# Kernel optimization log

Measured on AMD Instinct MI355X. Metric: run time of the kernel, lower is better.

## Reference

```python
import jax, jax.numpy as jnp
import numpy as np

# ---- HashGrid config (tcnn defaults from module __init__) ----
N_LEVELS = 6
F = 2                      # n_features_per_level
T = 2 ** 19                # hashmap size
BASE = 16                  # base_resolution, per_level_scale=2.0
_RES = [BASE * (2 ** l) for l in range(N_LEVELS)]          # 16..512
_SIZES = [min(r ** 3, T) for r in _RES]                    # dense if grid fits
_OFFSETS = [0] + list(np.cumsum(_SIZES))
TOTAL_ENTRIES = int(_OFFSETS[-1])
_PRIMES = (1, 2654435761, 805459861)
BOX_R = 1.0
DIM_H = 64
DIM_IN = 3 + N_LEVELS * F


def hash_encode(xn, grid):
    """Multi-res hash-grid encoding. xn: [N,3] in [0,1]; grid: [TOTAL_ENTRIES, F]."""
    feats = []
    for l in range(N_LEVELS):
        res, size, off = _RES[l], _SIZES[l], _OFFSETS[l]
        dense = (res ** 3) <= T
        pos = xn * jnp.float32(res - 1) + 0.5          # tcnn: scale*x + 0.5
        pg = jnp.floor(pos)
        frac = pos - pg                                # [N,3]
        pgi = pg.astype(jnp.uint32)
        acc = jnp.zeros((xn.shape[0], F), xn.dtype)
        for corner in range(8):                        # trilinear, 8 corners
            cb = jnp.array([(corner >> d) & 1 for d in range(3)], dtype=jnp.uint32)
            c = pgi + cb                               # [N,3] corner coords
            w = jnp.prod(jnp.where(cb == 1, frac, 1.0 - frac), axis=-1)  # [N]
            if dense:
                c = jnp.minimum(c, jnp.uint32(res - 1))
                idx = c[:, 0] + c[:, 1] * jnp.uint32(res) + c[:, 2] * jnp.uint32(res * res)
            else:
                idx = ((c[:, 0] * jnp.uint32(_PRIMES[0]))
                       ^ (c[:, 1] * jnp.uint32(_PRIMES[1]))
                       ^ (c[:, 2] * jnp.uint32(_PRIMES[2]))) % jnp.uint32(size)
            acc = acc + w[:, None] * grid[jnp.uint32(off) + idx]
        feats.append(acc)
    return jnp.concatenate(feats, axis=-1)             # [N, 12]


def setup_inputs() -> dict:
    key = jax.random.key(0)
    k0, k1, k2 = jax.random.split(key, 3)
    N = 2_097_152
    x = jax.random.uniform(k0, (N, 3), jnp.float32, -1.0, 1.0)
    grid = jax.random.uniform(k1, (TOTAL_ENTRIES, F), jnp.float32, -1e-2, 1e-2)
    W0 = jax.random.normal(k2, (DIM_IN, DIM_H), jnp.float32) * float(np.sqrt(2.0 / DIM_H))
    b0 = jnp.zeros((DIM_H,), jnp.float32)
    W1 = jnp.full((DIM_H, 1), float(np.sqrt(np.pi / DIM_H)), jnp.float32)
    b1 = jnp.full((1,), -1.0, jnp.float32)             # -init_radius
    return {"x": x, "grid": grid, "W0": W0, "b0": b0, "W1": W1, "b1": b1}


def reference(x, grid, W0, b0, W1, b1):
    xn = (x + BOX_R) / (2.0 * BOX_R)                   # normalize to [0,1]
    f = hash_encode(xn, grid)                          # [N,12]
    h = jnp.concatenate([x, f], axis=-1)               # [N,15]
    h = jax.nn.relu(h @ W0 + b0)                       # [N,64]
    return h @ W1 + b1                                 # [N,1] scalar level s
```

## Files before the change

kernel.cpp:

```cpp
#include <hip/hip_runtime.h>


#define HP1 2654435761u
#define HP2 805459861u
#define HMASK ((1u << 19) - 1u)

typedef float v2f __attribute__((ext_vector_type(2)));

static __device__ __forceinline__ unsigned umin_(unsigned a, unsigned b) {
    return a < b ? a : b;
}

static __device__ __forceinline__ unsigned f2bf(float f) {
    unsigned u = __float_as_uint(f);
    return (u + 0x7fffu + ((u >> 16) & 1u)) >> 16;
}
static __device__ __forceinline__ float bf2f_lo(unsigned p) {
    return __uint_as_float((p & 0xffffu) << 16);
}
static __device__ __forceinline__ float bf2f_hi(unsigned p) {
    return __uint_as_float(p & 0xffff0000u);
}

static __device__ __forceinline__ v2f vmax0(v2f s) {
#if __has_builtin(__builtin_elementwise_max)
    return __builtin_elementwise_max(s, (v2f)0.0f);
#else
    v2f r; r.x = fmaxf(s.x, 0.0f); r.y = fmaxf(s.y, 0.0f); return r;
#endif
}

static __device__ __forceinline__ void hash_body(
    const float* __restrict__ x, const float2* __restrict__ tab,
    unsigned* __restrict__ feat, float scale, int N, int bid)
{
    const int gid = bid * 256 + threadIdx.x;
    if (gid >= N) return;

    const float px = __builtin_nontemporal_load(x + 3 * gid + 0);
    const float py = __builtin_nontemporal_load(x + 3 * gid + 1);
    const float pz = __builtin_nontemporal_load(x + 3 * gid + 2);

    const float p0 = fmaf((px + 1.0f) * 0.5f, scale, 0.5f);
    const float p1 = fmaf((py + 1.0f) * 0.5f, scale, 0.5f);
    const float p2 = fmaf((pz + 1.0f) * 0.5f, scale, 0.5f);
    const float g0 = floorf(p0), g1 = floorf(p1), g2 = floorf(p2);
    const float f0 = p0 - g0, f1 = p1 - g1, f2 = p2 - g2;
    const unsigned i0 = (unsigned)g0, i1 = (unsigned)g1, i2 = (unsigned)g2;

    const float wx[2] = {1.0f - f0, f0};
    const float wy[2] = {1.0f - f1, f1};
    const float wz[2] = {1.0f - f2, f2};
    const unsigned hy[2] = {i1 * HP1, (i1 + 1u) * HP1};
    const unsigned hz[2] = {i2 * HP2, (i2 + 1u) * HP2};

    float2 v0[4], v1[4];
    #pragma unroll
    for (int c = 0; c < 4; ++c) {
        const unsigned m = hy[c & 1] ^ hz[(c >> 1) & 1];
        const unsigned e0 = (i0 ^ m) & HMASK;
        const float4 q = *reinterpret_cast<const float4*>(
            reinterpret_cast<const float*>(tab) + 2u * (e0 & ~1u));
        const float2 qlo = make_float2(q.x, q.y);
        const float2 qhi = make_float2(q.z, q.w);
        const bool hi = (e0 & 1u) != 0u;
        v0[c] = hi ? qhi : qlo;
        v1[c] = hi ? qlo : qhi;
    }
    if (i0 & 1u) {
        #pragma unroll
        for (int c = 0; c < 4; ++c) {
            const unsigned e1 =
                ((i0 + 1u) ^ hy[c & 1] ^ hz[(c >> 1) & 1]) & HMASK;
            v1[c] = tab[e1];
        }
    }

    float a0 = 0.0f, a1 = 0.0f;
    #pragma unroll
    for (int c = 0; c < 4; ++c) {
        const float wyz = wy[c & 1] * wz[(c >> 1) & 1];
        const float w0 = wyz * wx[0], w1 = wyz * wx[1];
        a0 = fmaf(w0, v0[c].x, a0);
        a1 = fmaf(w0, v0[c].y, a1);
        a0 = fmaf(w1, v1[c].x, a0);
        a1 = fmaf(w1, v1[c].y, a1);
    }
    __builtin_nontemporal_store(f2bf(a0) | (f2bf(a1) << 16), feat + gid);
}

__global__ __launch_bounds__(256) void hash3_prep_kernel(
    const float* __restrict__ x, const float2* __restrict__ gtab,
    unsigned* __restrict__ feat0, int N,
    float* __restrict__ wt, unsigned* __restrict__ packed,
    unsigned* __restrict__ A2, unsigned* __restrict__ B2,
    const float* __restrict__ W0, const float* __restrict__ b0,
    const float* __restrict__ W1, const float* __restrict__ b1)
{
    const int nh = (int)gridDim.x - 64;
    if ((int)blockIdx.x >= nh) {
        const int pb = (int)blockIdx.x - nh;
        for (int t = pb * 256 + threadIdx.x; t < 36864; t += 64 * 256) {
            const float2 e = gtab[t];
            packed[t] = f2bf(e.x) | (f2bf(e.y) << 16);
        }
        const float2* g2 = gtab + 36864u;
        for (int t = pb * 256 + threadIdx.x; t < 262144; t += 64 * 256) {
            const float2 e = g2[t];
            A2[t] = f2bf(e.x) | (f2bf(e.y) << 16);
            const int xc = t & 63;
            const float2 en = g2[(xc == 63) ? t : t + 1];
            B2[t] = f2bf(en.x) | (f2bf(en.y) << 16);
        }
        if (pb == 0) {
            for (int t = threadIdx.x; t < 1024; t += 256) {
                const int j = t >> 4, i = t & 15;
                wt[t] = (i == 15) ? b0[j] : W0[i * 64 + j];
            }
            if (threadIdx.x < 64) wt[1024 + threadIdx.x] = W1[threadIdx.x];
            if (threadIdx.x == 0) wt[1088] = b1[0];
        }
        return;
    }
    hash_body(x, gtab + 299008u, feat0, 127.0f, N, (int)blockIdx.x);
}

__global__ __launch_bounds__(256) void hash_level_kernel(
    const float* __restrict__ x, const float2* __restrict__ tab,
    unsigned* __restrict__ feat, float scale, int N)
{
    hash_body(x, tab, feat, scale, N, (int)blockIdx.x);
}

static __device__ __forceinline__ void dense_level(
    const float2* __restrict__ tab, unsigned res,
    float xn0, float xn1, float xn2, float& o0, float& o1)
{
    const float scale = (float)(res - 1);
    const float p0 = fmaf(xn0, scale, 0.5f);
    const float p1 = fmaf(xn1, scale, 0.5f);
    const float p2 = fmaf(xn2, scale, 0.5f);
    const float g0 = floorf(p0), g1 = floorf(p1), g2 = floorf(p2);
    const float f0 = p0 - g0, f1 = p1 - g1, f2 = p2 - g2;
    const unsigned i0 = (unsigned)g0, i1 = (unsigned)g1, i2 = (unsigned)g2;

    const unsigned rm1 = res - 1u;
    const unsigned cx[2] = {umin_(i0, rm1), umin_(i0 + 1u, rm1)};
    const unsigned cy[2] = {umin_(i1, rm1) * res, umin_(i1 + 1u, rm1) * res};
    const unsigned cz[2] = {umin_(i2, rm1) * res * res,
                            umin_(i2 + 1u, rm1) * res * res};
    const float wx[2] = {1.0f - f0, f0};
    const float wy[2] = {1.0f - f1, f1};
    const float wz[2] = {1.0f - f2, f2};

    float a0 = 0.0f, a1 = 0.0f;
    #pragma unroll
    for (int c = 0; c < 8; ++c) {
        const int bx = c & 1, by = (c >> 1) & 1, bz = (c >> 2) & 1;
        const unsigned idx = cx[bx] + cy[by] + cz[bz];
        const float w = wx[bx] * wy[by] * wz[bz];
        const float2 v = tab[idx];
        a0 = fmaf(w, v.x, a0);
        a1 = fmaf(w, v.y, a1);
    }
    o0 = a0;
    o1 = a1;
}

static __device__ __forceinline__ void dense_level2_pk(
    const unsigned* __restrict__ A2, const unsigned* __restrict__ B2,
    float xn0, float xn1, float xn2, float& o0, float& o1)
{
    const float p0 = fmaf(xn0, 63.0f, 0.5f);
    const float p1 = fmaf(xn1, 63.0f, 0.5f);
    const float p2 = fmaf(xn2, 63.0f, 0.5f);
    const float g0 = floorf(p0), g1 = floorf(p1), g2 = floorf(p2);
    const float f0 = p0 - g0, f1 = p1 - g1, f2 = p2 - g2;
    const unsigned i0 = (unsigned)g0, i1 = (unsigned)g1, i2 = (unsigned)g2;

    const unsigned cx0 = umin_(i0, 63u);
    const unsigned cy[2] = {umin_(i1, 63u) * 64u, umin_(i1 + 1u, 63u) * 64u};
    const unsigned cz[2] = {umin_(i2, 63u) * 4096u,
                            umin_(i2 + 1u, 63u) * 4096u};
    const float wx[2] = {1.0f - f0, f0};
    const float wy[2] = {1.0f - f1, f1};
    const float wz[2] = {1.0f - f2, f2};

    const unsigned* tsel = (cx0 & 1u) ? B2 : A2;
    const unsigned xb = cx0 & ~1u;

    float a0 = 0.0f, a1 = 0.0f;
    #pragma unroll
    for (int c = 0; c < 4; ++c) {
        const int by = c & 1, bz = (c >> 1) & 1;
        const uint2 q = *reinterpret_cast<const uint2*>(
            tsel + xb + cy[by] + cz[bz]);
        const float wyz = wy[by] * wz[bz];
        const float w0 = wyz * wx[0], w1 = wyz * wx[1];
        a0 = fmaf(w0, bf2f_lo(q.x), a0);
        a1 = fmaf(w0, bf2f_hi(q.x), a1);
        a0 = fmaf(w1, bf2f_lo(q.y), a0);
        a1 = fmaf(w1, bf2f_hi(q.y), a1);
    }
    o0 = a0;
    o1 = a1;
}

static __device__ __forceinline__ void dense_level_lds(
    const unsigned* __restrict__ sPk, unsigned off, unsigned res,
    float xn0, float xn1, float xn2, float& o0, float& o1)
{
    const float scale = (float)(res - 1);
    const float p0 = fmaf(xn0, scale, 0.5f);
    const float p1 = fmaf(xn1, scale, 0.5f);
    const float p2 = fmaf(xn2, scale, 0.5f);
    const float g0 = floorf(p0), g1 = floorf(p1), g2 = floorf(p2);
    const float f0 = p0 - g0, f1 = p1 - g1, f2 = p2 - g2;
    const unsigned i0 = (unsigned)g0, i1 = (unsigned)g1, i2 = (unsigned)g2;

    const unsigned rm1 = res - 1u;
    const unsigned cx[2] = {umin_(i0, rm1), umin_(i0 + 1u, rm1)};
    const unsigned cy[2] = {umin_(i1, rm1) * res, umin_(i1 + 1u, rm1) * res};
    const unsigned cz[2] = {umin_(i2, rm1) * res * res,
                            umin_(i2 + 1u, rm1) * res * res};
    const float wx[2] = {1.0f - f0, f0};
    const float wy[2] = {1.0f - f1, f1};
    const float wz[2] = {1.0f - f2, f2};

    float a0 = 0.0f, a1 = 0.0f;
    #pragma unroll
    for (int c = 0; c < 8; ++c) {
        const int bx = c & 1, by = (c >> 1) & 1, bz = (c >> 2) & 1;
        const unsigned p = sPk[off + cx[bx] + cy[by] + cz[bz]];
        const float w = wx[bx] * wy[by] * wz[bz];
        a0 = fmaf(w, bf2f_lo(p), a0);
        a1 = fmaf(w, bf2f_hi(p), a1);
    }
    o0 = a0;
    o1 = a1;
}

template<int BLOCK, bool L1LDS>
__global__ __launch_bounds__(BLOCK, 4) void dense_mlp_kernel(
    const float* __restrict__ x,
    const float* __restrict__ grid,
    const unsigned* __restrict__ feat,
    const float* __restrict__ wt,
    const unsigned* __restrict__ packed,
    const unsigned* __restrict__ A2,
    const unsigned* __restrict__ B2,
    float* __restrict__ out, int N)
{
    extern __shared__ unsigned sPk[];
    const int tid = threadIdx.x;

    const int nstage = L1LDS ? 36864 : 4096;
    for (int t = tid; t < nstage; t += BLOCK)
        sPk[t] = packed[t];
    __syncthreads();

    const int base = blockIdx.x * (BLOCK * 4) + tid;
    const float2* gtab = (const float2*)grid;

    v2f hp[2][16];

    #pragma unroll
    for (int k = 0; k < 4; ++k) {
        const int g = base + BLOCK * k;
        const int gs = (g < N) ? g : 0;
        const int p = k >> 1, lane = k & 1;

        const float px = __builtin_nontemporal_load(x + 3 * gs + 0);
        const float py = __builtin_nontemporal_load(x + 3 * gs + 1);
        const float pz = __builtin_nontemporal_load(x + 3 * gs + 2);
        const float xn0 = (px + 1.0f) * 0.5f;
        const float xn1 = (py + 1.0f) * 0.5f;
        const float xn2 = (pz + 1.0f) * 0.5f;

        hp[p][0][lane] = px; hp[p][1][lane] = py; hp[p][2][lane] = pz;
        hp[p][15][lane] = 1.0f;

        float t3, t4, t5, t6, t7, t8;
        dense_level_lds(sPk, 0u, 16u, xn0, xn1, xn2, t3, t4);
        if (L1LDS)
            dense_level_lds(sPk, 4096u, 32u, xn0, xn1, xn2, t5, t6);
        else
            dense_level(gtab + 4096u, 32u, xn0, xn1, xn2, t5, t6);
        dense_level2_pk(A2, B2, xn0, xn1, xn2, t7, t8);
        hp[p][3][lane] = t3; hp[p][4][lane] = t4;
        hp[p][5][lane] = t5; hp[p][6][lane] = t6;
        hp[p][7][lane] = t7; hp[p][8][lane] = t8;

        #pragma unroll
        for (int l = 0; l < 3; ++l) {
            const unsigned pk = __builtin_nontemporal_load(
                feat + (size_t)l * N + gs);
            hp[p][9 + 2 * l][lane]  = bf2f_lo(pk);
            hp[p][10 + 2 * l][lane] = bf2f_hi(pk);
        }
    }

    const float b1v = wt[1088];
    v2f o2[2];
    o2[0] = (v2f)b1v; o2[1] = (v2f)b1v;

    #pragma unroll 4
    for (int j = 0; j < 64; ++j) {
        float r[16];
        #pragma unroll
        for (int i = 0; i < 16; ++i)
            r[i] = wt[j * 16 + i];
        const float w1j = wt[1024 + j];
        #pragma unroll
        for (int p = 0; p < 2; ++p) {
            v2f s = (v2f)0.0f;
            #pragma unroll
            for (int i = 0; i < 16; ++i)
                s = hp[p][i] * r[i] + s;
            s = vmax0(s);
            o2[p] = s * w1j + o2[p];
        }
    }

    #pragma unroll
    for (int k = 0; k < 4; ++k) {
        const int g = base + BLOCK * k;
        if (g < N)
            __builtin_nontemporal_store(o2[k >> 1][k & 1], out + g);
    }
}

extern "C" void kernel_launch(void* const* d_in, const int* in_sizes, int n_in,
                              void* d_out, int out_size, void* d_ws, size_t ws_size,
                              hipStream_t stream) {
    const float* x    = (const float*)d_in[0];
    const float* grid = (const float*)d_in[1];
    const float* W0   = (const float*)d_in[2];
    const float* b0   = (const float*)d_in[3];
    const float* W1   = (const float*)d_in[4];
    const float* b1   = (const float*)d_in[5];
    float* out = (float*)d_out;

    const int N = in_sizes[0] / 3;
    const int blocks1 = (N + 255) / 256;

    const float2* gtab = (const float2*)grid;

    auto align256 = [](size_t v) { return (v + 255) & ~(size_t)255; };
    size_t off = 0;
    const size_t feat_off = off; off += align256((size_t)3 * N * 4);
    const size_t wt_off   = off; off += align256(1089 * 4);
    const size_t pk_off   = off; off += align256(36864 * 4);
    const size_t a2_off   = off; off += align256(262144 * 4);
    const size_t b2_off   = off; off += align256(262144 * 4);
    (void)ws_size;

    unsigned* feat   = (unsigned*)((char*)d_ws + feat_off);
    float*    wt     = (float*)((char*)d_ws + wt_off);
    unsigned* packed = (unsigned*)((char*)d_ws + pk_off);
    unsigned* A2     = (unsigned*)((char*)d_ws + a2_off);
    unsigned* B2     = (unsigned*)((char*)d_ws + b2_off);

    hash3_prep_kernel<<<blocks1 + 64, 256, 0, stream>>>(
        x, gtab, feat + (size_t)0 * N, N, wt, packed, A2, B2, W0, b0, W1, b1);
    hash_level_kernel<<<blocks1, 256, 0, stream>>>(x, gtab + 823296u,
                                                   feat + (size_t)1 * N, 255.0f, N);
    hash_level_kernel<<<blocks1, 256, 0, stream>>>(x, gtab + 1347584u,
                                                   feat + (size_t)2 * N, 511.0f, N);

    const size_t bigShm = 36864u * 4u;
    const void* bigK =
        reinterpret_cast<const void*>(&dense_mlp_kernel<1024, true>);
    (void)hipFuncSetAttribute(bigK,
        hipFuncAttributeMaxDynamicSharedMemorySize, (int)bigShm);
    bool big = false;
    hipFuncAttributes fa{};
    if (hipFuncGetAttributes(&fa, bigK) == hipSuccess)
        big = ((size_t)fa.maxDynamicSharedSizeBytes >= bigShm);

    if (big) {
        const int blocksB = (N + 4095) / 4096;
        dense_mlp_kernel<1024, true><<<blocksB, 1024, bigShm, stream>>>(
            x, (const float*)grid, feat, wt, packed, A2, B2, out, N);
    } else {
        const int blocksF = (N + 1023) / 1024;
        dense_mlp_kernel<256, false><<<blocksF, 256, 4096u * 4u, stream>>>(
            x, (const float*)grid, feat, wt, packed, A2, B2, out, N);
    }
}
```

Before: 369.9 us.

## Pack hashed level tables to bf16 and gather eight corners individually

A prep kernel now converts the three hashed level tables (2^19 entries each) into packed bf16 pairs, halving the table footprint so more of it stays in cache during random gathers. The hash kernels then do eight independent 4-byte gathers per point instead of paired float4 loads with a conditional second pass, and the first hash level no longer shares a launch with the prep work. The cost is an extra read-and-convert pass over about 12 MB of table on every call and serialising prep before hashing. There is also a small precision loss from storing table values in bf16.

```diff
diff --git a/kernel.cpp b/kernel.cpp
--- a/kernel.cpp
+++ b/kernel.cpp
@@ -30,11 +30,49 @@
 #endif
 }
 
-static __device__ __forceinline__ void hash_body(
-    const float* __restrict__ x, const float2* __restrict__ tab,
-    unsigned* __restrict__ feat, float scale, int N, int bid)
-{
-    const int gid = bid * 256 + threadIdx.x;
+__global__ __launch_bounds__(256) void prep_kernel(
+    const float2* __restrict__ gtab,
+    float* __restrict__ wt, unsigned* __restrict__ packed,
+    unsigned* __restrict__ A2, unsigned* __restrict__ B2,
+    unsigned* __restrict__ pk345,
+    const float* __restrict__ W0, const float* __restrict__ b0,
+    const float* __restrict__ W1, const float* __restrict__ b1)
+{
+    const int stride = (int)gridDim.x * 256;
+    const int t0 = (int)blockIdx.x * 256 + threadIdx.x;
+
+    for (int t = t0; t < 36864; t += stride) {
+        const float2 e = gtab[t];
+        packed[t] = f2bf(e.x) | (f2bf(e.y) << 16);
+    }
+    const float2* g2 = gtab + 36864u;
+    for (int t = t0; t < 262144; t += stride) {
+        const float2 e = g2[t];
+        A2[t] = f2bf(e.x) | (f2bf(e.y) << 16);
+        const int xc = t & 63;
+        const float2 en = g2[(xc == 63) ? t : t + 1];
+        B2[t] = f2bf(en.x) | (f2bf(en.y) << 16);
+    }
+    const float2* gh = gtab + 299008u;
+    for (int t = t0; t < 3 * 524288; t += stride) {
+        const float2 e = gh[t];
+        pk345[t] = f2bf(e.x) | (f2bf(e.y) << 16);
+    }
+    if (blockIdx.x == 0) {
+        for (int t = threadIdx.x; t < 1024; t += 256) {
+            const int j = t >> 4, i = t & 15;
+            wt[t] = (i == 15) ? b0[j] : W0[i * 64 + j];
+        }
+        if (threadIdx.x < 64) wt[1024 + threadIdx.x] = W1[threadIdx.x];
+        if (threadIdx.x == 0) wt[1088] = b1[0];
+    }
+}
+
+__global__ __launch_bounds__(256) void hash_level_kernel(
+    const float* __restrict__ x, const unsigned* __restrict__ tab,
+    unsigned* __restrict__ feat, float scale, int N)
+{
+    const int gid = (int)blockIdx.x * 256 + threadIdx.x;
     if (gid >= N) return;
 
     const float px = __builtin_nontemporal_load(x + 3 * gid + 0);
@@ -51,85 +89,29 @@
     const float wx[2] = {1.0f - f0, f0};
     const float wy[2] = {1.0f - f1, f1};
     const float wz[2] = {1.0f - f2, f2};
+    const unsigned hx[2] = {i0, i0 + 1u};
     const unsigned hy[2] = {i1 * HP1, (i1 + 1u) * HP1};
     const unsigned hz[2] = {i2 * HP2, (i2 + 1u) * HP2};
 
-    float2 v0[4], v1[4];
-    #pragma unroll
-    for (int c = 0; c < 4; ++c) {
-        const unsigned m = hy[c & 1] ^ hz[(c >> 1) & 1];
-        const unsigned e0 = (i0 ^ m) & HMASK;
-        const float4 q = *reinterpret_cast<const float4*>(
-            reinterpret_cast<const float*>(tab) + 2u * (e0 & ~1u));
-        const float2 qlo = make_float2(q.x, q.y);
-        const float2 qhi = make_float2(q.z, q.w);
-        const bool hi = (e0 & 1u) != 0u;
-        v0[c] = hi ? qhi : qlo;
-        v1[c] = hi ? qlo : qhi;
-    }
-    if (i0 & 1u) {
-        #pragma unroll
-        for (int c = 0; c < 4; ++c) {
-            const unsigned e1 =
-                ((i0 + 1u) ^ hy[c & 1] ^ hz[(c >> 1) & 1]) & HMASK;
-            v1[c] = tab[e1];
-        }
-    }
+    unsigned idx[8];
+    float w[8];
+    #pragma unroll
+    for (int c = 0; c < 8; ++c) {
+        const int bx = c & 1, by = (c >> 1) & 1, bz = (c >> 2) & 1;
+        idx[c] = (hx[bx] ^ hy[by] ^ hz[bz]) & HMASK;
+        w[c] = wx[bx] * wy[by] * wz[bz];
+    }
+    unsigned v[8];
+    #pragma unroll
+    for (int c = 0; c < 8; ++c) v[c] = tab[idx[c]];
 
     float a0 = 0.0f, a1 = 0.0f;
     #pragma unroll
-    for (int c = 0; c < 4; ++c) {
-        const float wyz = wy[c & 1] * wz[(c >> 1) & 1];
-        const float w0 = wyz * wx[0], w1 = wyz * wx[1];
-        a0 = fmaf(w0, v0[c].x, a0);
-        a1 = fmaf(w0, v0[c].y, a1);
-        a0 = fmaf(w1, v1[c].x, a0);
-        a1 = fmaf(w1, v1[c].y, a1);
+    for (int c = 0; c < 8; ++c) {
+        a0 = fmaf(w[c], bf2f_lo(v[c]), a0);
+        a1 = fmaf(w[c], bf2f_hi(v[c]), a1);
     }
     __builtin_nontemporal_store(f2bf(a0) | (f2bf(a1) << 16), feat + gid);
-}
-
-__global__ __launch_bounds__(256) void hash3_prep_kernel(
-    const float* __restrict__ x, const float2* __restrict__ gtab,
-    unsigned* __restrict__ feat0, int N,
-    float* __restrict__ wt, unsigned* __restrict__ packed,
-    unsigned* __restrict__ A2, unsigned* __restrict__ B2,
-    const float* __restrict__ W0, const float* __restrict__ b0,
-    const float* __restrict__ W1, const float* __restrict__ b1)
-{
-    const int nh = (int)gridDim.x - 64;
-    if ((int)blockIdx.x >= nh) {
-        const int pb = (int)blockIdx.x - nh;
-        for (int t = pb * 256 + threadIdx.x; t < 36864; t += 64 * 256) {
-            const float2 e = gtab[t];
-            packed[t] = f2bf(e.x) | (f2bf(e.y) << 16);
-        }
-        const float2* g2 = gtab + 36864u;
-        for (int t = pb * 256 + threadIdx.x; t < 262144; t += 64 * 256) {
-            const float2 e = g2[t];
-            A2[t] = f2bf(e.x) | (f2bf(e.y) << 16);
-            const int xc = t & 63;
-            const float2 en = g2[(xc == 63) ? t : t + 1];
-            B2[t] = f2bf(en.x) | (f2bf(en.y) << 16);
-        }
-        if (pb == 0) {
-            for (int t = threadIdx.x; t < 1024; t += 256) {
-                const int j = t >> 4, i = t & 15;
-                wt[t] = (i == 15) ? b0[j] : W0[i * 64 + j];
-            }
-            if (threadIdx.x < 64) wt[1024 + threadIdx.x] = W1[threadIdx.x];
-            if (threadIdx.x == 0) wt[1088] = b1[0];
-        }
-        return;
-    }
-    hash_body(x, gtab + 299008u, feat0, 127.0f, N, (int)blockIdx.x);
-}
-
-__global__ __launch_bounds__(256) void hash_level_kernel(
-    const float* __restrict__ x, const float2* __restrict__ tab,
-    unsigned* __restrict__ feat, float scale, int N)
-{
-    hash_body(x, tab, feat, scale, N, (int)blockIdx.x);
 }
 
 static __device__ __forceinline__ void dense_level(
@@ -353,6 +335,7 @@
     const size_t pk_off   = off; off += align256(36864 * 4);
     const size_t a2_off   = off; off += align256(262144 * 4);
     const size_t b2_off   = off; off += align256(262144 * 4);
+    const size_t h_off    = off; off += align256((size_t)3 * 524288 * 4);
     (void)ws_size;
 
     unsigned* feat   = (unsigned*)((char*)d_ws + feat_off);
@@ -360,13 +343,17 @@
     unsigned* packed = (unsigned*)((char*)d_ws + pk_off);
     unsigned* A2     = (unsigned*)((char*)d_ws + a2_off);
     unsigned* B2     = (unsigned*)((char*)d_ws + b2_off);
-
-    hash3_prep_kernel<<<blocks1 + 64, 256, 0, stream>>>(
-        x, gtab, feat + (size_t)0 * N, N, wt, packed, A2, B2, W0, b0, W1, b1);
-    hash_level_kernel<<<blocks1, 256, 0, stream>>>(x, gtab + 823296u,
-                                                   feat + (size_t)1 * N, 255.0f, N);
-    hash_level_kernel<<<blocks1, 256, 0, stream>>>(x, gtab + 1347584u,
-                                                   feat + (size_t)2 * N, 511.0f, N);
+    unsigned* pk345  = (unsigned*)((char*)d_ws + h_off);
+
+    prep_kernel<<<512, 256, 0, stream>>>(gtab, wt, packed, A2, B2, pk345,
+                                         W0, b0, W1, b1);
+
+    hash_level_kernel<<<blocks1, 256, 0, stream>>>(
+        x, pk345 + (size_t)0 * 524288, feat + (size_t)0 * N, 127.0f, N);
+    hash_level_kernel<<<blocks1, 256, 0, stream>>>(
+        x, pk345 + (size_t)1 * 524288, feat + (size_t)1 * N, 255.0f, N);
+    hash_level_kernel<<<blocks1, 256, 0, stream>>>(
+        x, pk345 + (size_t)2 * 524288, feat + (size_t)2 * N, 511.0f, N);
 
     const size_t bigShm = 36864u * 4u;
     const void* bigK =
```

Result: faster. 315.4 us (-14.7%).

## Fuse finest hash level into MLP kernel and simplify hash gathers

Applied to the files above, without the earlier changes.

Removes the separate kernel launch for the 512-resolution hash level. That level is now gathered directly inside the final dense+MLP kernel, which avoids writing and re-reading a bf16 feature plane and one extra launch. The standalone hash-level kernel's paired float4 gather trick is replaced by eight plain float2 gathers issued all up front. The MLP loop is also split per point pair. In exchange, the fused kernel carries more register pressure and random global loads, and it may get lower occupancy. The 256-res level now does more load instructions.

```diff
diff --git a/kernel.cpp b/kernel.cpp
--- a/kernel.cpp
+++ b/kernel.cpp
@@ -51,40 +51,27 @@
     const float wx[2] = {1.0f - f0, f0};
     const float wy[2] = {1.0f - f1, f1};
     const float wz[2] = {1.0f - f2, f2};
+    const unsigned hx[2] = {i0, i0 + 1u};
     const unsigned hy[2] = {i1 * HP1, (i1 + 1u) * HP1};
     const unsigned hz[2] = {i2 * HP2, (i2 + 1u) * HP2};
 
-    float2 v0[4], v1[4];
-    #pragma unroll
-    for (int c = 0; c < 4; ++c) {
-        const unsigned m = hy[c & 1] ^ hz[(c >> 1) & 1];
-        const unsigned e0 = (i0 ^ m) & HMASK;
-        const float4 q = *reinterpret_cast<const float4*>(
-            reinterpret_cast<const float*>(tab) + 2u * (e0 & ~1u));
-        const float2 qlo = make_float2(q.x, q.y);
-        const float2 qhi = make_float2(q.z, q.w);
-        const bool hi = (e0 & 1u) != 0u;
-        v0[c] = hi ? qhi : qlo;
-        v1[c] = hi ? qlo : qhi;
-    }
-    if (i0 & 1u) {
-        #pragma unroll
-        for (int c = 0; c < 4; ++c) {
-            const unsigned e1 =
-                ((i0 + 1u) ^ hy[c & 1] ^ hz[(c >> 1) & 1]) & HMASK;
-            v1[c] = tab[e1];
-        }
-    }
+    unsigned idx[8];
+    float w[8];
+    #pragma unroll
+    for (int c = 0; c < 8; ++c) {
+        const int bx = c & 1, by = (c >> 1) & 1, bz = (c >> 2) & 1;
+        idx[c] = (hx[bx] ^ hy[by] ^ hz[bz]) & HMASK;
+        w[c] = wx[bx] * wy[by] * wz[bz];
+    }
+    float2 v[8];
+    #pragma unroll
+    for (int c = 0; c < 8; ++c) v[c] = tab[idx[c]];
 
     float a0 = 0.0f, a1 = 0.0f;
     #pragma unroll
-    for (int c = 0; c < 4; ++c) {
-        const float wyz = wy[c & 1] * wz[(c >> 1) & 1];
-        const float w0 = wyz * wx[0], w1 = wyz * wx[1];
-        a0 = fmaf(w0, v0[c].x, a0);
-        a1 = fmaf(w0, v0[c].y, a1);
-        a0 = fmaf(w1, v1[c].x, a0);
-        a1 = fmaf(w1, v1[c].y, a1);
+    for (int c = 0; c < 8; ++c) {
+        a0 = fmaf(w[c], v[c].x, a0);
+        a1 = fmaf(w[c], v[c].y, a1);
     }
     __builtin_nontemporal_store(f2bf(a0) | (f2bf(a1) << 16), feat + gid);
 }
@@ -167,6 +154,40 @@
     o1 = a1;
 }
 
+static __device__ __forceinline__ void dense_level_lds(
+    const unsigned* __restrict__ sPk, unsigned off, unsigned res,
+    float xn0, float xn1, float xn2, float& o0, float& o1)
+{
+    const float scale = (float)(res - 1);
+    const float p0 = fmaf(xn0, scale, 0.5f);
+    const float p1 = fmaf(xn1, scale, 0.5f);
+    const float p2 = fmaf(xn2, scale, 0.5f);
+    const float g0 = floorf(p0), g1 = floorf(p1), g2 = floorf(p2);
+    const float f0 = p0 - g0, f1 = p1 - g1, f2 = p2 - g2;
+    const unsigned i0 = (unsigned)g0, i1 = (unsigned)g1, i2 = (unsigned)g2;
+
+    const unsigned rm1 = res - 1u;
+    const unsigned cx[2] = {umin_(i0, rm1), umin_(i0 + 1u, rm1)};
+    const unsigned cy[2] = {umin_(i1, rm1) * res, umin_(i1 + 1u, rm1) * res};
+    const unsigned cz[2] = {umin_(i2, rm1) * res * res,
+                            umin_(i2 + 1u, rm1) * res * res};
+    const float wx[2] = {1.0f - f0, f0};
+    const float wy[2] = {1.0f - f1, f1};
+    const float wz[2] = {1.0f - f2, f2};
+
+    float a0 = 0.0f, a1 = 0.0f;
+    #pragma unroll
+    for (int c = 0; c < 8; ++c) {
+        const int bx = c & 1, by = (c >> 1) & 1, bz = (c >> 2) & 1;
+        const unsigned p = sPk[off + cx[bx] + cy[by] + cz[bz]];
+        const float w = wx[bx] * wy[by] * wz[bz];
+        a0 = fmaf(w, bf2f_lo(p), a0);
+        a1 = fmaf(w, bf2f_hi(p), a1);
+    }
+    o0 = a0;
+    o1 = a1;
+}
+
 static __device__ __forceinline__ void dense_level2_pk(
     const unsigned* __restrict__ A2, const unsigned* __restrict__ B2,
     float xn0, float xn1, float xn2, float& o0, float& o1)
@@ -206,42 +227,69 @@
     o1 = a1;
 }
 
-static __device__ __forceinline__ void dense_level_lds(
-    const unsigned* __restrict__ sPk, unsigned off, unsigned res,
-    float xn0, float xn1, float xn2, float& o0, float& o1)
-{
-    const float scale = (float)(res - 1);
-    const float p0 = fmaf(xn0, scale, 0.5f);
-    const float p1 = fmaf(xn1, scale, 0.5f);
-    const float p2 = fmaf(xn2, scale, 0.5f);
+static __device__ __forceinline__ void hash5_pt(
+    const float2* __restrict__ tab, float xn0, float xn1, float xn2,
+    float& o0, float& o1)
+{
+    const float p0 = fmaf(xn0, 511.0f, 0.5f);
+    const float p1 = fmaf(xn1, 511.0f, 0.5f);
+    const float p2 = fmaf(xn2, 511.0f, 0.5f);
     const float g0 = floorf(p0), g1 = floorf(p1), g2 = floorf(p2);
     const float f0 = p0 - g0, f1 = p1 - g1, f2 = p2 - g2;
     const unsigned i0 = (unsigned)g0, i1 = (unsigned)g1, i2 = (unsigned)g2;
 
-    const unsigned rm1 = res - 1u;
-    const unsigned cx[2] = {umin_(i0, rm1), umin_(i0 + 1u, rm1)};
-    const unsigned cy[2] = {umin_(i1, rm1) * res, umin_(i1 + 1u, rm1) * res};
-    const unsigned cz[2] = {umin_(i2, rm1) * res * res,
-                            umin_(i2 + 1u, rm1) * res * res};
     const float wx[2] = {1.0f - f0, f0};
     const float wy[2] = {1.0f - f1, f1};
     const float wz[2] = {1.0f - f2, f2};
+    const unsigned hx[2] = {i0, i0 + 1u};
+    const unsigned hy[2] = {i1 * HP1, (i1 + 1u) * HP1};
+    const unsigned hz[2] = {i2 * HP2, (i2 + 1u) * HP2};
+
+    unsigned idx[8];
+    float w[8];
+    #pragma unroll
+    for (int c = 0; c < 8; ++c) {
+        const int bx = c & 1, by = (c >> 1) & 1, bz = (c >> 2) & 1;
+        idx[c] = (hx[bx] ^ hy[by] ^ hz[bz]) & HMASK;
+        w[c] = wx[bx] * wy[by] * wz[bz];
+    }
+    float2 v[8];
+    #pragma unroll
+    for (int c = 0; c < 8; ++c) v[c] = tab[idx[c]];
 
     float a0 = 0.0f, a1 = 0.0f;
     #pragma unroll
     for (int c = 0; c < 8; ++c) {
-        const int bx = c & 1, by = (c >> 1) & 1, bz = (c >> 2) & 1;
-        const unsigned p = sPk[off + cx[bx] + cy[by] + cz[bz]];
-        const float w = wx[bx] * wy[by] * wz[bz];
-        a0 = fmaf(w, bf2f_lo(p), a0);
-        a1 = fmaf(w, bf2f_hi(p), a1);
+        a0 = fmaf(w[c], v[c].x, a0);
+        a1 = fmaf(w[c], v[c].y, a1);
     }
     o0 = a0;
     o1 = a1;
 }
 
+static __device__ __forceinline__ v2f mlp_pair(
+    const float* __restrict__ wt, const v2f* __restrict__ hp)
+{
+    v2f o2 = (v2f)wt[1088];
+    #pragma unroll 4
+    for (int j = 0; j < 64; ++j) {
+        float r[16];
+        #pragma unroll
+        for (int i = 0; i < 16; ++i)
+            r[i] = wt[j * 16 + i];
+        const float w1j = wt[1024 + j];
+        v2f s = (v2f)0.0f;
+        #pragma unroll
+        for (int i = 0; i < 16; ++i)
+            s = hp[i] * r[i] + s;
+        s = vmax0(s);
+        o2 = s * w1j + o2;
+    }
+    return o2;
+}
+
 template<int BLOCK, bool L1LDS>
-__global__ __launch_bounds__(BLOCK, 4) void dense_mlp_kernel(
+__global__ __launch_bounds__(BLOCK, 4) void fused5_mlp_kernel(
     const float* __restrict__ x,
     const float* __restrict__ grid,
     const unsigned* __restrict__ feat,
@@ -261,6 +309,7 @@
 
     const int base = blockIdx.x * (BLOCK * 4) + tid;
     const float2* gtab = (const float2*)grid;
+    const float2* tab5 = gtab + 1347584u;
 
     v2f hp[2][16];
 
@@ -279,6 +328,10 @@
 
         hp[p][0][lane] = px; hp[p][1][lane] = py; hp[p][2][lane] = pz;
         hp[p][15][lane] = 1.0f;
+
+        float h5a, h5b;
+        hash5_pt(tab5, xn0, xn1, xn2, h5a, h5b);
+        hp[p][13][lane] = h5a; hp[p][14][lane] = h5b;
 
         float t3, t4, t5, t6, t7, t8;
         dense_level_lds(sPk, 0u, 16u, xn0, xn1, xn2, t3, t4);
@@ -292,7 +345,7 @@
         hp[p][7][lane] = t7; hp[p][8][lane] = t8;
 
         #pragma unroll
-        for (int l = 0; l < 3; ++l) {
+        for (int l = 0; l < 2; ++l) {
             const unsigned pk = __builtin_nontemporal_load(
                 feat + (size_t)l * N + gs);
             hp[p][9 + 2 * l][lane]  = bf2f_lo(pk);
@@ -300,27 +353,9 @@
         }
     }
 
-    const float b1v = wt[1088];
     v2f o2[2];
-    o2[0] = (v2f)b1v; o2[1] = (v2f)b1v;
-
-    #pragma unroll 4
-    for (int j = 0; j < 64; ++j) {
-        float r[16];
-        #pragma unroll
-        for (int i = 0; i < 16; ++i)
-            r[i] = wt[j * 16 + i];
-        const float w1j = wt[1024 + j];
-        #pragma unroll
-        for (int p = 0; p < 2; ++p) {
-            v2f s = (v2f)0.0f;
-            #pragma unroll
-            for (int i = 0; i < 16; ++i)
-                s = hp[p][i] * r[i] + s;
-            s = vmax0(s);
-            o2[p] = s * w1j + o2[p];
-        }
-    }
+    o2[0] = mlp_pair(wt, hp[0]);
+    o2[1] = mlp_pair(wt, hp[1]);
 
     #pragma unroll
     for (int k = 0; k < 4; ++k) {
@@ -348,7 +383,7 @@
 
     auto align256 = [](size_t v) { return (v + 255) & ~(size_t)255; };
     size_t off = 0;
-    const size_t feat_off = off; off += align256((size_t)3 * N * 4);
+    const size_t feat_off = off; off += align256((size_t)2 * N * 4);
     const size_t wt_off   = off; off += align256(1089 * 4);
     const size_t pk_off   = off; off += align256(36864 * 4);
     const size_t a2_off   = off; off += align256(262144 * 4);
@@ -363,14 +398,12 @@
 
     hash3_prep_kernel<<<blocks1 + 64, 256, 0, stream>>>(
         x, gtab, feat + (size_t)0 * N, N, wt, packed, A2, B2, W0, b0, W1, b1);
-    hash_level_kernel<<<blocks1, 256, 0, stream>>>(x, gtab + 823296u,
-                                                   feat + (size_t)1 * N, 255.0f, N);
-    hash_level_kernel<<<blocks1, 256, 0, stream>>>(x, gtab + 1347584u,
-                                                   feat + (size_t)2 * N, 511.0f, N);
+    hash_level_kernel<<<blocks1, 256, 0, stream>>>(
+        x, gtab + 823296u, feat + (size_t)1 * N, 255.0f, N);
 
     const size_t bigShm = 36864u * 4u;
     const void* bigK =
-        reinterpret_cast<const void*>(&dense_mlp_kernel<1024, true>);
+        reinterpret_cast<const void*>(&fused5_mlp_kernel<1024, true>);
     (void)hipFuncSetAttribute(bigK,
         hipFuncAttributeMaxDynamicSharedMemorySize, (int)bigShm);
     bool big = false;
@@ -380,11 +413,11 @@
 
     if (big) {
         const int blocksB = (N + 4095) / 4096;
-        dense_mlp_kernel<1024, true><<<blocksB, 1024, bigShm, stream>>>(
+        fused5_mlp_kernel<1024, true><<<blocksB, 1024, bigShm, stream>>>(
             x, (const float*)grid, feat, wt, packed, A2, B2, out, N);
     } else {
         const int blocksF = (N + 1023) / 1024;
-        dense_mlp_kernel<256, false><<<blocksF, 256, 4096u * 4u, stream>>>(
+        fused5_mlp_kernel<256, false><<<blocksF, 256, 4096u * 4u, stream>>>(
             x, (const float*)grid, feat, wt, packed, A2, B2, out, N);
     }
 }
```

New measurement: 365.4 us. No clear change (-1.2%).
